# Kernel tuning notes

Measured on AMD Instinct MI355X. Metric: run time of the kernel, lower is better.

## Reference

```python
import jax, jax.numpy as jnp
import numpy as np

B, T, D = 64, 2048, 256


def setup_inputs() -> dict:
    key = jax.random.key(0)
    k0, k1, k2, k3 = jax.random.split(key, 4)
    x0 = jax.random.normal(k0, (B, D), dtype=jnp.float32)
    I = jax.random.normal(k1, (B, T, D), dtype=jnp.float32)
    # Scale transition matrix so spectral norm < 1 (stable 2048-step recurrence),
    # mimicking eW = expm((W - I)*dt/tau) which is contractive for stable W.
    eW = jax.random.normal(k2, (D, D), dtype=jnp.float32) * (0.9 / np.sqrt(D))
    W_inv_eW = jax.random.normal(k3, (D, D), dtype=jnp.float32) * (1.0 / np.sqrt(D))
    return {"x0": x0, "I": I, "eW": eW, "W_inv_eW": W_inv_eW}


def reference(x0, I, eW, W_inv_eW):
    # x[:,0]=x0; x[:,t] = x[:,t-1] @ eW.T + I[:,t-1] @ W_inv_eW.T
    u = jnp.einsum('btd,sd->bts', I, W_inv_eW)  # [B, T, D], precompute input drive

    def step(x, u_t):
        x_new = x @ eW.T + u_t  # [B, D]
        return x_new, x_new

    # only u[:, :T-1] is consumed (x[:,t] uses I[:,t-1])
    _, xs = jax.lax.scan(step, x0, jnp.swapaxes(u[:, :-1], 0, 1))  # xs: [T-1, B, D]
    x = jnp.concatenate([x0[:, None, :], jnp.swapaxes(xs, 0, 1)], axis=1)  # [B, T, D]
    return x
```

## Files before the change

kernel.cpp:

```cpp
#include <hip/hip_runtime.h>
#include <stdint.h>
#include <stddef.h>


#define BATCH 64
#define TLEN 2048
#define DDIM 256
#define CHUNK 32
#define NCHUNK 64

typedef __attribute__((ext_vector_type(8))) short short8;
typedef __attribute__((ext_vector_type(4))) float f32x4;

#define MFMA16(a, b, c) __builtin_amdgcn_mfma_f32_16x16x32_bf16((a), (b), (c), 0, 0, 0)
#define PIN8(x) asm volatile("" : "+v"(x))

__device__ __forceinline__ uint16_t f2bf(float f) {
  union { float f; uint32_t u; } v; v.f = f;
  return (uint16_t)((v.u + 0x7fffu + ((v.u >> 16) & 1u)) >> 16);
}
__device__ __forceinline__ float bf2f(uint16_t h) {
  union { uint32_t u; float f; } v; v.u = ((uint32_t)h) << 16;
  return v.f;
}

__device__ __forceinline__ void split8(const float* fv, short8& hi, short8& lo) {
#pragma unroll
  for (int j = 0; j < 8; ++j) {
    uint16_t hb = f2bf(fv[j]);
    hi[j] = (short)hb;
    lo[j] = (short)f2bf(fv[j] - bf2f(hb));
  }
}

__device__ __forceinline__ uint32_t swz(int row) {
  return ((uint32_t)((row & 7) << 4)) ^ ((uint32_t)(((row >> 3) & 1) << 7));
}

__device__ __forceinline__ void wg_barrier() {
  __builtin_amdgcn_sched_barrier(0);
  asm volatile("s_waitcnt lgkmcnt(0)" ::: "memory");
  __builtin_amdgcn_s_barrier();
  asm volatile("" ::: "memory");
  __builtin_amdgcn_sched_barrier(0);
}

#define WS_A_HI   (0)
#define WS_A_LO   (128 * 1024)
#define WS_WB_HI  (256 * 1024)
#define WS_WB_LO  (384 * 1024)
#define WS_M1F    (512 * 1024)
#define WS_M1_HI  (768 * 1024)
#define WS_M1_LO  (896 * 1024)
#define WS_M2F    (1024 * 1024)
#define WS_M2_HI  (1280 * 1024)
#define WS_M2_LO  (1408 * 1024)
#define WS_M3F    (1536 * 1024)
#define WS_M3_HI  (1792 * 1024)
#define WS_M3_LO  (1920 * 1024)
#define WS_ATF    (2048 * 1024)
#define WS_S      (2560 * 1024)
#define WS_Y      (6656 * 1024)

__global__ void k_split(const float* __restrict__ eW, const float* __restrict__ Wi,
                        uint16_t* __restrict__ Ah, uint16_t* __restrict__ Al,
                        uint16_t* __restrict__ Wh, uint16_t* __restrict__ Wl,
                        float* __restrict__ AtF) {
  int idx = blockIdx.x * blockDim.x + threadIdx.x;
  if (idx < 65536) {
    float v = eW[idx];
    uint16_t h = f2bf(v);
    Ah[idx] = h;
    Al[idx] = f2bf(v - bf2f(h));
    AtF[(idx & 255) * 256 + (idx >> 8)] = v;
  } else if (idx < 131072) {
    int i = idx - 65536;
    float v = Wi[i];
    uint16_t h = f2bf(v);
    Wh[i] = h;
    Wl[i] = f2bf(v - bf2f(h));
  }
}

__global__ __launch_bounds__(512, 1) void k_u(const float* __restrict__ I,
                                              const uint16_t* __restrict__ Wh,
                                              const uint16_t* __restrict__ Wl,
                                              float* __restrict__ out) {
  const int tid = threadIdx.x;
  const int w = tid >> 6, l = tid & 63, l15 = l & 15, quad = l >> 4;
  const int ns = w * 32;
  __shared__ __align__(16) uint16_t sIh[2][4096];
  __shared__ __align__(16) uint16_t sIl[2][4096];

  short8 bh[2][8], bl[2][8];
#pragma unroll
  for (int nf = 0; nf < 2; ++nf)
#pragma unroll
    for (int ks = 0; ks < 8; ++ks) {
      const int off = (ns + nf * 16 + l15) * 256 + ks * 32 + quad * 8;
      bh[nf][ks] = *reinterpret_cast<const short8*>(Wh + off);
      bl[nf][ks] = *reinterpret_cast<const short8*>(Wl + off);
      PIN8(bh[nf][ks]);
      PIN8(bl[nf][ks]);
    }

  const int srow = tid >> 5;
  const int sc0 = (tid & 31) * 8;
  const uint32_t wbyte = ((uint32_t)(srow * 512 + sc0 * 2)) ^ swz(srow);

  float ra[8], rb[8], rc[8], rd[8];
  auto loadI = [&](int tl, float (&dst)[8]) {
    const int b = tl >> 7, tt = tl & 127;
    const float* src = I + ((size_t)b * TLEN + tt * 16 + srow) * DDIM + sc0;
    *reinterpret_cast<f32x4*>(&dst[0]) = *reinterpret_cast<const f32x4*>(src);
    *reinterpret_cast<f32x4*>(&dst[4]) = *reinterpret_cast<const f32x4*>(src + 4);
  };

  auto do_tile = [&](int tl, float (&cur)[8], float (&pf)[8], int q, bool pre) {
    if (pre) loadI(tl + 512, pf);
    short8 hi, lo;
    split8(cur, hi, lo);
    *reinterpret_cast<short8*>(reinterpret_cast<char*>(sIh[q]) + wbyte) = hi;
    *reinterpret_cast<short8*>(reinterpret_cast<char*>(sIl[q]) + wbyte) = lo;
    wg_barrier();
    const int b = tl >> 7, tt = tl & 127;
    f32x4 acc0 = {0.f, 0.f, 0.f, 0.f}, acc1 = {0.f, 0.f, 0.f, 0.f};
#pragma unroll
    for (int ks = 0; ks < 8; ++ks) {
      uint32_t rbyte = ((uint32_t)(l15 * 512 + ks * 64 + quad * 16)) ^ swz(l15);
      short8 ih = *reinterpret_cast<const short8*>((const char*)sIh[q] + rbyte);
      short8 il = *reinterpret_cast<const short8*>((const char*)sIl[q] + rbyte);
      acc0 = MFMA16(ih, bh[0][ks], acc0);
      acc0 = MFMA16(il, bh[0][ks], acc0);
      acc0 = MFMA16(ih, bl[0][ks], acc0);
      acc1 = MFMA16(ih, bh[1][ks], acc1);
      acc1 = MFMA16(il, bh[1][ks], acc1);
      acc1 = MFMA16(ih, bl[1][ks], acc1);
    }
#pragma unroll
    for (int nf = 0; nf < 2; ++nf)
#pragma unroll
      for (int r = 0; r < 4; ++r) {
        int trow = tt * 16 + quad * 4 + r;
        if (trow <= TLEN - 2) {
          int col = ns + nf * 16 + l15;
          out[((size_t)b * TLEN + trow + 1) * DDIM + col] = (nf ? acc1 : acc0)[r];
        }
      }
  };

  const int tl0 = blockIdx.x;
  loadI(tl0, ra);
  loadI(tl0 + 256, rb);
#pragma unroll 1
  for (int it = 0; it < 32; it += 4) {
    do_tile(tl0 + (it + 0) * 256, ra, rc, 0, it + 2 < 32);
    do_tile(tl0 + (it + 1) * 256, rb, rd, 1, it + 3 < 32);
    do_tile(tl0 + (it + 2) * 256, rc, ra, 0, it + 4 < 32);
    do_tile(tl0 + (it + 3) * 256, rd, rb, 1, it + 5 < 32);
  }
}

__global__ __launch_bounds__(1024) void k_scan(const int pass,
                                               const uint16_t* __restrict__ Ah,
                                               const uint16_t* __restrict__ Al,
                                               float* __restrict__ xu,
                                               const float* __restrict__ Y,
                                               float* __restrict__ S) {
  const int tid = threadIdx.x;
  const int w = tid >> 6, l = tid & 63, l15 = l & 15, quad = l >> 4;
  const int ns = w * 16;
  const int c = blockIdx.x >> 2;
  const int rg = blockIdx.x & 3;
  __shared__ __align__(16) uint16_t sh[2][4096];
  __shared__ __align__(16) uint16_t sl[2][4096];

  const int t0 = c * CHUNK;
  const int nsteps = (t0 + CHUNK <= TLEN - 1) ? CHUNK : (TLEN - 1 - t0);

  float u0[4], u1[4], u2[4], u3[4], fin[4];
#pragma unroll
  for (int j = 0; j < 4; ++j) { u0[j] = 0.f; u1[j] = 0.f; u2[j] = 0.f; u3[j] = 0.f; fin[j] = 0.f; }

  auto issue_u = [&](int i, float (&dst)[4]) {
    if (i > nsteps) return;
#pragma unroll
    for (int r = 0; r < 4; ++r) {
      int b = rg * 16 + quad * 4 + r;
      dst[r] = xu[((size_t)b * TLEN + t0 + i) * DDIM + ns + l15];
    }
  };
  issue_u(1, u0);
  issue_u(2, u1);
  issue_u(3, u2);
  issue_u(4, u3);

  short8 fAh[8], fAl[8];
#pragma unroll
  for (int ks = 0; ks < 8; ++ks) {
    const int off = (ns + l15) * 256 + ks * 32 + quad * 8;
    fAh[ks] = *reinterpret_cast<const short8*>(Ah + off);
    fAl[ks] = *reinterpret_cast<const short8*>(Al + off);
    PIN8(fAh[ks]);
    PIN8(fAl[ks]);
  }

  for (int i = tid; i < 4096; i += 1024) {
    int row = i >> 8, k = i & 255;
    float v;
    if (pass == 1)
      v = 0.0f;
    else {
      v = Y[((size_t)c * 64 + rg * 16 + row) * DDIM + k];
      if (c == 0) xu[((size_t)(rg * 16 + row) * TLEN) * DDIM + k] = v;
    }
    uint16_t hb = f2bf(v);
    uint16_t lb = f2bf(v - bf2f(hb));
    uint32_t byte = ((uint32_t)(row * 512 + k * 2)) ^ swz(row);
    *(uint16_t*)((char*)sh[0] + byte) = hb;
    *(uint16_t*)((char*)sl[0] + byte) = lb;
  }
  wg_barrier();

  int p = 0;
  auto step = [&](int i, float (&ucur)[4]) {
    f32x4 acc = {0.f, 0.f, 0.f, 0.f};
#pragma unroll
    for (int ks = 0; ks < 8; ++ks) {
      uint32_t byte = ((uint32_t)(l15 * 512 + ks * 64 + quad * 16)) ^ swz(l15);
      short8 xh = *reinterpret_cast<const short8*>((const char*)sh[p] + byte);
      short8 xl = *reinterpret_cast<const short8*>((const char*)sl[p] + byte);
      acc = MFMA16(xh, fAh[ks], acc);
      acc = MFMA16(xl, fAh[ks], acc);
      acc = MFMA16(xh, fAl[ks], acc);
    }
#pragma unroll
    for (int r = 0; r < 4; ++r) fin[r] = acc[r] + ucur[r];
    issue_u(i + 4, ucur);
    if (pass == 2) {
#pragma unroll
      for (int r = 0; r < 4; ++r) {
        int b = rg * 16 + quad * 4 + r;
        xu[((size_t)b * TLEN + t0 + i) * DDIM + ns + l15] = fin[r];
      }
    }
    if (i < nsteps) {
#pragma unroll
      for (int r = 0; r < 4; ++r) {
        int row = quad * 4 + r, col = ns + l15;
        float v = fin[r];
        uint16_t hb = f2bf(v);
        uint16_t lb = f2bf(v - bf2f(hb));
        uint32_t byte = ((uint32_t)(row * 512 + col * 2)) ^ swz(row);
        *(uint16_t*)((char*)sh[p ^ 1] + byte) = hb;
        *(uint16_t*)((char*)sl[p ^ 1] + byte) = lb;
      }
      wg_barrier();
      p ^= 1;
    }
  };

  int i = 1;
  for (; i + 3 <= nsteps; i += 4) {
    step(i, u0);
    step(i + 1, u1);
    step(i + 2, u2);
    step(i + 3, u3);
  }
  if (i <= nsteps) { step(i, u0); ++i; }
  if (i <= nsteps) { step(i, u1); ++i; }
  if (i <= nsteps) { step(i, u2); ++i; }

  if (pass == 1) {
#pragma unroll
    for (int r = 0; r < 4; ++r) {
      int row = quad * 4 + r, col = ns + l15;
      S[((size_t)c * 64 + rg * 16 + row) * DDIM + col] = fin[r];
    }
  }
}

__global__ __launch_bounds__(512) void k_mm256(const float* __restrict__ Af,
                                               const uint16_t* __restrict__ Bh,
                                               const uint16_t* __restrict__ Bl,
                                               float* __restrict__ Of,
                                               uint16_t* __restrict__ Oh,
                                               uint16_t* __restrict__ Ol) {
  const int mf = blockIdx.x;
  const int tid = threadIdx.x;
  const int w = tid >> 6, l = tid & 63, l15 = l & 15, quad = l >> 4;
  const int ns = w * 32;
  f32x4 acc[2];
  acc[0] = {0.f, 0.f, 0.f, 0.f};
  acc[1] = {0.f, 0.f, 0.f, 0.f};

#pragma unroll
  for (int ks = 0; ks < 8; ++ks) {
    const float* ap = Af + (size_t)(mf * 16 + l15) * 256 + ks * 32 + quad * 8;
    f32x4 f0 = *reinterpret_cast<const f32x4*>(ap);
    f32x4 f1 = *reinterpret_cast<const f32x4*>(ap + 4);
    float fv[8] = {f0[0], f0[1], f0[2], f0[3], f1[0], f1[1], f1[2], f1[3]};
    short8 ah, al8;
    split8(fv, ah, al8);
#pragma unroll
    for (int nf = 0; nf < 2; ++nf) {
      const int off = (ns + nf * 16 + l15) * 256 + ks * 32 + quad * 8;
      short8 bhf = *reinterpret_cast<const short8*>(Bh + off);
      short8 blf = *reinterpret_cast<const short8*>(Bl + off);
      acc[nf] = MFMA16(ah, bhf, acc[nf]);
      acc[nf] = MFMA16(al8, bhf, acc[nf]);
      acc[nf] = MFMA16(ah, blf, acc[nf]);
    }
  }
#pragma unroll
  for (int nf = 0; nf < 2; ++nf)
#pragma unroll
    for (int r = 0; r < 4; ++r) {
      int row = mf * 16 + quad * 4 + r;
      int col = ns + nf * 16 + l15;
      float v = acc[nf][r];
      Of[(size_t)row * 256 + col] = v;
      uint16_t hb = f2bf(v);
      Oh[(size_t)col * 256 + row] = hb;
      Ol[(size_t)col * 256 + row] = f2bf(v - bf2f(hb));
    }
}

__global__ __launch_bounds__(512) void k_bnd(const float* __restrict__ x0,
                                             const float* __restrict__ S,
                                             const uint16_t* __restrict__ M1h, const uint16_t* __restrict__ M1l,
                                             const uint16_t* __restrict__ M2h, const uint16_t* __restrict__ M2l,
                                             const uint16_t* __restrict__ M3h, const uint16_t* __restrict__ M3l,
                                             float* __restrict__ Y) {
  const int c = blockIdx.x;
  const int tid = threadIdx.x;
  const int w = tid >> 6, l = tid & 63, l15 = l & 15, quad = l >> 4;
  const int ns = w * 32;
  f32x4 acc[4][2];
  const float* Tc = (c == 0) ? x0 : (S + (size_t)(c - 1) * 64 * 256);
#pragma unroll
  for (int mf = 0; mf < 4; ++mf)
#pragma unroll
    for (int nf = 0; nf < 2; ++nf)
#pragma unroll
      for (int r = 0; r < 4; ++r)
        acc[mf][nf][r] = Tc[(size_t)(mf * 16 + quad * 4 + r) * 256 + ns + nf * 16 + l15];

  for (int j = 1; j <= 3; ++j) {
    int k = c - j;
    if (k < 0) break;
    const float* Tp = (k == 0) ? x0 : (S + (size_t)(k - 1) * 64 * 256);
    const uint16_t* Bh = (j == 1) ? M1h : (j == 2) ? M2h : M3h;
    const uint16_t* Bl = (j == 1) ? M1l : (j == 2) ? M2l : M3l;
#pragma unroll
    for (int mf = 0; mf < 4; ++mf) {
#pragma unroll
      for (int ks = 0; ks < 8; ++ks) {
        const float* ap = Tp + (size_t)(mf * 16 + l15) * 256 + ks * 32 + quad * 8;
        f32x4 f0 = *reinterpret_cast<const f32x4*>(ap);
        f32x4 f1 = *reinterpret_cast<const f32x4*>(ap + 4);
        float fv[8] = {f0[0], f0[1], f0[2], f0[3], f1[0], f1[1], f1[2], f1[3]};
        short8 ah, al8;
        split8(fv, ah, al8);
#pragma unroll
        for (int nf = 0; nf < 2; ++nf) {
          const int off = (ns + nf * 16 + l15) * 256 + ks * 32 + quad * 8;
          short8 bhf = *reinterpret_cast<const short8*>(Bh + off);
          short8 blf = *reinterpret_cast<const short8*>(Bl + off);
          acc[mf][nf] = MFMA16(ah, bhf, acc[mf][nf]);
          acc[mf][nf] = MFMA16(al8, bhf, acc[mf][nf]);
          acc[mf][nf] = MFMA16(ah, blf, acc[mf][nf]);
        }
      }
    }
  }
#pragma unroll
  for (int mf = 0; mf < 4; ++mf)
#pragma unroll
    for (int nf = 0; nf < 2; ++nf)
#pragma unroll
      for (int r = 0; r < 4; ++r)
        Y[(size_t)c * 64 * 256 + (size_t)(mf * 16 + quad * 4 + r) * 256 + ns + nf * 16 + l15] =
            acc[mf][nf][r];
}

extern "C" void kernel_launch(void* const* d_in, const int* in_sizes, int n_in,
                              void* d_out, int out_size, void* d_ws, size_t ws_size,
                              hipStream_t stream) {
  (void)in_sizes; (void)n_in; (void)out_size; (void)ws_size;
  const float* x0 = (const float*)d_in[0];
  const float* I  = (const float*)d_in[1];
  const float* eW = (const float*)d_in[2];
  const float* Wi = (const float*)d_in[3];
  float* out = (float*)d_out;
  char* ws = (char*)d_ws;

  uint16_t* Ah  = (uint16_t*)(ws + WS_A_HI);
  uint16_t* Al  = (uint16_t*)(ws + WS_A_LO);
  uint16_t* Wh  = (uint16_t*)(ws + WS_WB_HI);
  uint16_t* Wl  = (uint16_t*)(ws + WS_WB_LO);
  float*    M1f = (float*)(ws + WS_M1F);
  uint16_t* M1h = (uint16_t*)(ws + WS_M1_HI);
  uint16_t* M1l = (uint16_t*)(ws + WS_M1_LO);
  float*    M2f = (float*)(ws + WS_M2F);
  uint16_t* M2h = (uint16_t*)(ws + WS_M2_HI);
  uint16_t* M2l = (uint16_t*)(ws + WS_M2_LO);
  float*    M3f = (float*)(ws + WS_M3F);
  uint16_t* M3h = (uint16_t*)(ws + WS_M3_HI);
  uint16_t* M3l = (uint16_t*)(ws + WS_M3_LO);
  float*    AtF = (float*)(ws + WS_ATF);
  float*    S   = (float*)(ws + WS_S);
  float*    Y   = (float*)(ws + WS_Y);

  k_split<<<512, 256, 0, stream>>>(eW, Wi, Ah, Al, Wh, Wl, AtF);
  k_u<<<256, 512, 0, stream>>>(I, Wh, Wl, out);
  k_mm256<<<16, 512, 0, stream>>>(AtF, Ah, Al, M2f, M2h, M2l);
  k_mm256<<<16, 512, 0, stream>>>(M2f, M2h, M2l, M3f, M3h, M3l);
  k_mm256<<<16, 512, 0, stream>>>(M3f, M3h, M3l, M2f, M2h, M2l);
  k_mm256<<<16, 512, 0, stream>>>(M2f, M2h, M2l, M3f, M3h, M3l);
  k_mm256<<<16, 512, 0, stream>>>(M3f, M3h, M3l, M1f, M1h, M1l);
  k_mm256<<<16, 512, 0, stream>>>(M1f, M1h, M1l, M2f, M2h, M2l);
  k_mm256<<<16, 512, 0, stream>>>(M2f, M1h, M1l, M3f, M3h, M3l);
  k_scan<<<256, 1024, 0, stream>>>(1, Ah, Al, out, Y, S);
  k_bnd<<<64, 512, 0, stream>>>(x0, S, M1h, M1l, M2h, M2l, M3h, M3l, Y);
  k_scan<<<256, 1024, 0, stream>>>(2, Ah, Al, out, Y, S);
}
```

Baseline: 340.1 us.

## Fuse matrix-power chain into one persistent kernel and widen input-projection blocks

The seven separate 256x256 matrix-product launches are merged into a single 16-block kernel that uses a global atomic-counter barrier between stages, removing per-launch overhead and gaps. The input-projection kernel moves to 1024 threads per block, with each wave owning 16 output columns instead of 32, so per-wave register use drops and more waves are resident. s_setprio hints are also added around the MFMA loops in both the projection and scan kernels. The spin barrier relies on all 16 blocks being co-resident, and the counter is reset inside the split kernel.

```diff
diff --git a/kernel.cpp b/kernel.cpp
--- a/kernel.cpp
+++ b/kernel.cpp
@@ -10,6 +10,7 @@
 #define NCHUNK 64
 
 typedef __attribute__((ext_vector_type(8))) short short8;
+typedef __attribute__((ext_vector_type(4))) short short4_t;
 typedef __attribute__((ext_vector_type(4))) float f32x4;
 
 #define MFMA16(a, b, c) __builtin_amdgcn_mfma_f32_16x16x32_bf16((a), (b), (c), 0, 0, 0)
@@ -59,14 +60,16 @@
 #define WS_M3_HI  (1792 * 1024)
 #define WS_M3_LO  (1920 * 1024)
 #define WS_ATF    (2048 * 1024)
+#define WS_CNT    (2304 * 1024)
 #define WS_S      (2560 * 1024)
 #define WS_Y      (6656 * 1024)
 
 __global__ void k_split(const float* __restrict__ eW, const float* __restrict__ Wi,
                         uint16_t* __restrict__ Ah, uint16_t* __restrict__ Al,
                         uint16_t* __restrict__ Wh, uint16_t* __restrict__ Wl,
-                        float* __restrict__ AtF) {
+                        float* __restrict__ AtF, unsigned int* __restrict__ cnt) {
   int idx = blockIdx.x * blockDim.x + threadIdx.x;
+  if (idx == 0) *cnt = 0u;
   if (idx < 65536) {
     float v = eW[idx];
     uint16_t h = f2bf(v);
@@ -82,71 +85,137 @@
   }
 }
 
-__global__ __launch_bounds__(512, 1) void k_u(const float* __restrict__ I,
-                                              const uint16_t* __restrict__ Wh,
-                                              const uint16_t* __restrict__ Wl,
-                                              float* __restrict__ out) {
+__global__ __launch_bounds__(512) void k_power(
+    const float* __restrict__ AtF, const uint16_t* __restrict__ Ah, const uint16_t* __restrict__ Al,
+    float* __restrict__ M1f, uint16_t* __restrict__ M1h, uint16_t* __restrict__ M1l,
+    float* __restrict__ M2f, uint16_t* __restrict__ M2h, uint16_t* __restrict__ M2l,
+    float* __restrict__ M3f, uint16_t* __restrict__ M3h, uint16_t* __restrict__ M3l,
+    unsigned int* __restrict__ cnt) {
+  const int mf = blockIdx.x;
   const int tid = threadIdx.x;
   const int w = tid >> 6, l = tid & 63, l15 = l & 15, quad = l >> 4;
   const int ns = w * 32;
+
+  auto mm = [&](const float* Af, const uint16_t* Bh, const uint16_t* Bl,
+                float* Of, uint16_t* Oh, uint16_t* Ol) {
+    f32x4 acc[2];
+    acc[0] = {0.f, 0.f, 0.f, 0.f};
+    acc[1] = {0.f, 0.f, 0.f, 0.f};
+#pragma unroll
+    for (int ks = 0; ks < 8; ++ks) {
+      const float* ap = Af + (size_t)(mf * 16 + l15) * 256 + ks * 32 + quad * 8;
+      f32x4 f0 = *reinterpret_cast<const f32x4*>(ap);
+      f32x4 f1 = *reinterpret_cast<const f32x4*>(ap + 4);
+      float fv[8] = {f0[0], f0[1], f0[2], f0[3], f1[0], f1[1], f1[2], f1[3]};
+      short8 ah, al8;
+      split8(fv, ah, al8);
+#pragma unroll
+      for (int nf = 0; nf < 2; ++nf) {
+        const int off = (ns + nf * 16 + l15) * 256 + ks * 32 + quad * 8;
+        short8 bhf = *reinterpret_cast<const short8*>(Bh + off);
+        short8 blf = *reinterpret_cast<const short8*>(Bl + off);
+        acc[nf] = MFMA16(ah, bhf, acc[nf]);
+        acc[nf] = MFMA16(al8, bhf, acc[nf]);
+        acc[nf] = MFMA16(ah, blf, acc[nf]);
+      }
+    }
+#pragma unroll
+    for (int nf = 0; nf < 2; ++nf)
+#pragma unroll
+      for (int r = 0; r < 4; ++r) {
+        int row = mf * 16 + quad * 4 + r;
+        int col = ns + nf * 16 + l15;
+        float v = acc[nf][r];
+        Of[(size_t)row * 256 + col] = v;
+        uint16_t hb = f2bf(v);
+        Oh[(size_t)col * 256 + row] = hb;
+        Ol[(size_t)col * 256 + row] = f2bf(v - bf2f(hb));
+      }
+  };
+
+  unsigned int target = 0;
+  auto gbar = [&]() {
+    __syncthreads();
+    target += 16;
+    if (tid == 0) {
+      __hip_atomic_fetch_add(cnt, 1u, __ATOMIC_RELEASE, __HIP_MEMORY_SCOPE_AGENT);
+      while (__hip_atomic_load(cnt, __ATOMIC_ACQUIRE, __HIP_MEMORY_SCOPE_AGENT) < target) {
+      }
+    }
+    __syncthreads();
+  };
+
+  mm(AtF, Ah, Al, M2f, M2h, M2l);    gbar();
+  mm(M2f, M2h, M2l, M3f, M3h, M3l);  gbar();
+  mm(M3f, M3h, M3l, M2f, M2h, M2l);  gbar();
+  mm(M2f, M2h, M2l, M3f, M3h, M3l);  gbar();
+  mm(M3f, M3h, M3l, M1f, M1h, M1l);  gbar();
+  mm(M1f, M1h, M1l, M2f, M2h, M2l);  gbar();
+  mm(M2f, M1h, M1l, M3f, M3h, M3l);
+}
+
+__global__ __launch_bounds__(1024, 1) void k_u(const float* __restrict__ I,
+                                               const uint16_t* __restrict__ Wh,
+                                               const uint16_t* __restrict__ Wl,
+                                               float* __restrict__ out) {
+  const int tid = threadIdx.x;
+  const int w = tid >> 6, l = tid & 63, l15 = l & 15, quad = l >> 4;
+  const int ns = w * 16;
   __shared__ __align__(16) uint16_t sIh[2][4096];
   __shared__ __align__(16) uint16_t sIl[2][4096];
 
-  short8 bh[2][8], bl[2][8];
-#pragma unroll
-  for (int nf = 0; nf < 2; ++nf)
-#pragma unroll
-    for (int ks = 0; ks < 8; ++ks) {
-      const int off = (ns + nf * 16 + l15) * 256 + ks * 32 + quad * 8;
-      bh[nf][ks] = *reinterpret_cast<const short8*>(Wh + off);
-      bl[nf][ks] = *reinterpret_cast<const short8*>(Wl + off);
-      PIN8(bh[nf][ks]);
-      PIN8(bl[nf][ks]);
-    }
-
-  const int srow = tid >> 5;
-  const int sc0 = (tid & 31) * 8;
+  short8 bh[8], bl[8];
+#pragma unroll
+  for (int ks = 0; ks < 8; ++ks) {
+    const int off = (ns + l15) * 256 + ks * 32 + quad * 8;
+    bh[ks] = *reinterpret_cast<const short8*>(Wh + off);
+    bl[ks] = *reinterpret_cast<const short8*>(Wl + off);
+    PIN8(bh[ks]);
+    PIN8(bl[ks]);
+  }
+
+  const int srow = tid >> 6;
+  const int sc0 = (tid & 63) * 4;
   const uint32_t wbyte = ((uint32_t)(srow * 512 + sc0 * 2)) ^ swz(srow);
 
-  float ra[8], rb[8], rc[8], rd[8];
-  auto loadI = [&](int tl, float (&dst)[8]) {
+  f32x4 ra, rb, rc, rd;
+  auto loadI = [&](int tl, f32x4& dst) {
     const int b = tl >> 7, tt = tl & 127;
-    const float* src = I + ((size_t)b * TLEN + tt * 16 + srow) * DDIM + sc0;
-    *reinterpret_cast<f32x4*>(&dst[0]) = *reinterpret_cast<const f32x4*>(src);
-    *reinterpret_cast<f32x4*>(&dst[4]) = *reinterpret_cast<const f32x4*>(src + 4);
-  };
-
-  auto do_tile = [&](int tl, float (&cur)[8], float (&pf)[8], int q, bool pre) {
+    dst = *reinterpret_cast<const f32x4*>(I + ((size_t)b * TLEN + tt * 16 + srow) * DDIM + sc0);
+  };
+
+  auto do_tile = [&](int tl, f32x4& cur, f32x4& pf, int q, bool pre) {
     if (pre) loadI(tl + 512, pf);
-    short8 hi, lo;
-    split8(cur, hi, lo);
-    *reinterpret_cast<short8*>(reinterpret_cast<char*>(sIh[q]) + wbyte) = hi;
-    *reinterpret_cast<short8*>(reinterpret_cast<char*>(sIl[q]) + wbyte) = lo;
+    short4_t hi4, lo4;
+#pragma unroll
+    for (int j = 0; j < 4; ++j) {
+      uint16_t hb = f2bf(cur[j]);
+      hi4[j] = (short)hb;
+      lo4[j] = (short)f2bf(cur[j] - bf2f(hb));
+    }
+    *reinterpret_cast<short4_t*>(reinterpret_cast<char*>(sIh[q]) + wbyte) = hi4;
+    *reinterpret_cast<short4_t*>(reinterpret_cast<char*>(sIl[q]) + wbyte) = lo4;
     wg_barrier();
     const int b = tl >> 7, tt = tl & 127;
-    f32x4 acc0 = {0.f, 0.f, 0.f, 0.f}, acc1 = {0.f, 0.f, 0.f, 0.f};
+    f32x4 acc = {0.f, 0.f, 0.f, 0.f};
+    __builtin_amdgcn_s_setprio(1);
 #pragma unroll
     for (int ks = 0; ks < 8; ++ks) {
       uint32_t rbyte = ((uint32_t)(l15 * 512 + ks * 64 + quad * 16)) ^ swz(l15);
       short8 ih = *reinterpret_cast<const short8*>((const char*)sIh[q] + rbyte);
       short8 il = *reinterpret_cast<const short8*>((const char*)sIl[q] + rbyte);
-      acc0 = MFMA16(ih, bh[0][ks], acc0);
-      acc0 = MFMA16(il, bh[0][ks], acc0);
-      acc0 = MFMA16(ih, bl[0][ks], acc0);
-      acc1 = MFMA16(ih, bh[1][ks], acc1);
-      acc1 = MFMA16(il, bh[1][ks], acc1);
-      acc1 = MFMA16(ih, bl[1][ks], acc1);
-    }
-#pragma unroll
-    for (int nf = 0; nf < 2; ++nf)
-#pragma unroll
-      for (int r = 0; r < 4; ++r) {
-        int trow = tt * 16 + quad * 4 + r;
-        if (trow <= TLEN - 2) {
-          int col = ns + nf * 16 + l15;
-          out[((size_t)b * TLEN + trow + 1) * DDIM + col] = (nf ? acc1 : acc0)[r];
-        }
-      }
+      acc = MFMA16(ih, bh[ks], acc);
+      acc = MFMA16(il, bh[ks], acc);
+      acc = MFMA16(ih, bl[ks], acc);
+    }
+    __builtin_amdgcn_s_setprio(0);
+#pragma unroll
+    for (int r = 0; r < 4; ++r) {
+      int trow = tt * 16 + quad * 4 + r;
+      if (trow <= TLEN - 2) {
+        out[((size_t)b * TLEN + trow + 1) * DDIM + ns + l15] = acc[r];
+      }
+    }
   };
 
   const int tl0 = blockIdx.x;
@@ -225,6 +294,7 @@
   int p = 0;
   auto step = [&](int i, float (&ucur)[4]) {
     f32x4 acc = {0.f, 0.f, 0.f, 0.f};
+    __builtin_amdgcn_s_setprio(1);
 #pragma unroll
     for (int ks = 0; ks < 8; ++ks) {
       uint32_t byte = ((uint32_t)(l15 * 512 + ks * 64 + quad * 16)) ^ swz(l15);
@@ -234,6 +304,7 @@
       acc = MFMA16(xl, fAh[ks], acc);
       acc = MFMA16(xh, fAl[ks], acc);
     }
+    __builtin_amdgcn_s_setprio(0);
 #pragma unroll
     for (int r = 0; r < 4; ++r) fin[r] = acc[r] + ucur[r];
     issue_u(i + 4, ucur);
@@ -278,52 +349,6 @@
       S[((size_t)c * 64 + rg * 16 + row) * DDIM + col] = fin[r];
     }
   }
-}
-
-__global__ __launch_bounds__(512) void k_mm256(const float* __restrict__ Af,
-                                               const uint16_t* __restrict__ Bh,
-                                               const uint16_t* __restrict__ Bl,
-                                               float* __restrict__ Of,
-                                               uint16_t* __restrict__ Oh,
-                                               uint16_t* __restrict__ Ol) {
-  const int mf = blockIdx.x;
-  const int tid = threadIdx.x;
-  const int w = tid >> 6, l = tid & 63, l15 = l & 15, quad = l >> 4;
-  const int ns = w * 32;
-  f32x4 acc[2];
-  acc[0] = {0.f, 0.f, 0.f, 0.f};
-  acc[1] = {0.f, 0.f, 0.f, 0.f};
-
-#pragma unroll
-  for (int ks = 0; ks < 8; ++ks) {
-    const float* ap = Af + (size_t)(mf * 16 + l15) * 256 + ks * 32 + quad * 8;
-    f32x4 f0 = *reinterpret_cast<const f32x4*>(ap);
-    f32x4 f1 = *reinterpret_cast<const f32x4*>(ap + 4);
-    float fv[8] = {f0[0], f0[1], f0[2], f0[3], f1[0], f1[1], f1[2], f1[3]};
-    short8 ah, al8;
-    split8(fv, ah, al8);
-#pragma unroll
-    for (int nf = 0; nf < 2; ++nf) {
-      const int off = (ns + nf * 16 + l15) * 256 + ks * 32 + quad * 8;
-      short8 bhf = *reinterpret_cast<const short8*>(Bh + off);
-      short8 blf = *reinterpret_cast<const short8*>(Bl + off);
-      acc[nf] = MFMA16(ah, bhf, acc[nf]);
-      acc[nf] = MFMA16(al8, bhf, acc[nf]);
-      acc[nf] = MFMA16(ah, blf, acc[nf]);
-    }
-  }
-#pragma unroll
-  for (int nf = 0; nf < 2; ++nf)
-#pragma unroll
-    for (int r = 0; r < 4; ++r) {
-      int row = mf * 16 + quad * 4 + r;
-      int col = ns + nf * 16 + l15;
-      float v = acc[nf][r];
-      Of[(size_t)row * 256 + col] = v;
-      uint16_t hb = f2bf(v);
-      Oh[(size_t)col * 256 + row] = hb;
-      Ol[(size_t)col * 256 + row] = f2bf(v - bf2f(hb));
-    }
 }
 
 __global__ __launch_bounds__(512) void k_bnd(const float* __restrict__ x0,
@@ -409,18 +434,14 @@
   uint16_t* M3h = (uint16_t*)(ws + WS_M3_HI);
   uint16_t* M3l = (uint16_t*)(ws + WS_M3_LO);
   float*    AtF = (float*)(ws + WS_ATF);
+  unsigned int* cnt = (unsigned int*)(ws + WS_CNT);
   float*    S   = (float*)(ws + WS_S);
   float*    Y   = (float*)(ws + WS_Y);
 
-  k_split<<<512, 256, 0, stream>>>(eW, Wi, Ah, Al, Wh, Wl, AtF);
-  k_u<<<256, 512, 0, stream>>>(I, Wh, Wl, out);
-  k_mm256<<<16, 512, 0, stream>>>(AtF, Ah, Al, M2f, M2h, M2l);
-  k_mm256<<<16, 512, 0, stream>>>(M2f, M2h, M2l, M3f, M3h, M3l);
-  k_mm256<<<16, 512, 0, stream>>>(M3f, M3h, M3l, M2f, M2h, M2l);
-  k_mm256<<<16, 512, 0, stream>>>(M2f, M2h, M2l, M3f, M3h, M3l);
-  k_mm256<<<16, 512, 0, stream>>>(M3f, M3h, M3l, M1f, M1h, M1l);
-  k_mm256<<<16, 512, 0, stream>>>(M1f, M1h, M1l, M2f, M2h, M2l);
-  k_mm256<<<16, 512, 0, stream>>>(M2f, M1h, M1l, M3f, M3h, M3l);
+  k_split<<<512, 256, 0, stream>>>(eW, Wi, Ah, Al, Wh, Wl, AtF, cnt);
+  k_power<<<16, 512, 0, stream>>>(AtF, Ah, Al, M1f, M1h, M1l, M2f, M2h, M2l,
+                                  M3f, M3h, M3l, cnt);
+  k_u<<<256, 1024, 0, stream>>>(I, Wh, Wl, out);
   k_scan<<<256, 1024, 0, stream>>>(1, Ah, Al, out, Y, S);
   k_bnd<<<64, 512, 0, stream>>>(x0, S, M1h, M1l, M2h, M2l, M3h, M3l, Y);
   k_scan<<<256, 1024, 0, stream>>>(2, Ah, Al, out, Y, S);
```

After: 342.3 us. Within noise of the previous version (+0.6%).
